# Kernel tuning notes

Measured on AMD Instinct MI355X. Metric: run time of the kernel, lower is better.

## Reference

```python
import jax, jax.numpy as jnp
import numpy as np

B, S, D = 4, 2048, 512
H = 8
HD = D // H  # 64


def setup_inputs() -> dict:
    key = jax.random.key(0)
    ks = jax.random.split(key, 11)
    scale = 1.0 / np.sqrt(D)
    inp = {
        "query": jax.random.normal(ks[0], (B, S, D), dtype=jnp.float32),
        "key": jax.random.normal(ks[1], (B, S, D), dtype=jnp.float32),
        "value": jax.random.normal(ks[2], (B, S, D), dtype=jnp.float32),
        "Wq": jax.random.normal(ks[3], (D, D), dtype=jnp.float32) * scale,
        "bq": jnp.zeros((D,), dtype=jnp.float32),
        "Wk": jax.random.normal(ks[4], (D, D), dtype=jnp.float32) * scale,
        "bk": jnp.zeros((D,), dtype=jnp.float32),
        "Wv": jax.random.normal(ks[5], (D, D), dtype=jnp.float32) * scale,
        "bv": jnp.zeros((D,), dtype=jnp.float32),
        "Wo": jax.random.normal(ks[6], (D, D), dtype=jnp.float32) * scale,
        "bo": jnp.zeros((D,), dtype=jnp.float32),
    }
    return inp


def reference(query, key, value, Wq, bq, Wk, bk, Wv, bv, Wo, bo):
    # Linear projections (torch Linear: x @ W.T + b)
    q = (query @ Wq.T + bq).reshape(B, -1, H, HD).transpose(0, 2, 1, 3)  # [B,H,Sq,HD]
    k = (key   @ Wk.T + bk).reshape(B, -1, H, HD).transpose(0, 2, 1, 3)  # [B,H,Sk,HD]
    v = (value @ Wv.T + bv).reshape(B, -1, H, HD).transpose(0, 2, 1, 3)  # [B,H,Sk,HD]

    # Chunked loop in original is mathematically identical to full attention
    scores = jnp.einsum('bhqd,bhkd->bhqk', q, k) / np.sqrt(HD)  # [B,H,Sq,Sk]
    attn = jax.nn.softmax(scores, axis=-1)
    out = jnp.einsum('bhqk,bhkd->bhqd', attn, v)  # [B,H,Sq,HD]
    out = out.transpose(0, 2, 1, 3).reshape(B, -1, D)  # [B,Sq,D]
    return out @ Wo.T + bo
```

## Files before the change

### kernel.cpp

```cpp
#include <hip/hip_runtime.h>
#include <hip/hip_bf16.h>

typedef __attribute__((ext_vector_type(8))) short bf16x8;
typedef __attribute__((ext_vector_type(4))) float f32x4;
typedef __attribute__((ext_vector_type(16))) float f32x16;
typedef __attribute__((ext_vector_type(4))) unsigned int u32x4;

#define MFMA16(a, b, c) __builtin_amdgcn_mfma_f32_16x16x32_bf16((a), (b), (c), 0, 0, 0)
#define MFMA32(a, b, c) __builtin_amdgcn_mfma_f32_32x32x16_bf16((a), (b), (c), 0, 0, 0)

static constexpr int BATCH = 4, S = 2048, DMODEL = 512, H = 8, HD = 64;
static constexpr int M = BATCH * S;

#define WAIT_VM(N) asm volatile("s_waitcnt vmcnt(" #N ")" ::: "memory")
#define WAIT_VM_LGKM(N) asm volatile("s_waitcnt vmcnt(" #N ") lgkmcnt(0)" ::: "memory")
#define SCHEDB() __builtin_amdgcn_sched_barrier(0)

__device__ __forceinline__ float rexp2(float x) {
  float r;
  asm("v_exp_f32 %0, %1" : "=v"(r) : "v"(x));
  return r;
}

__device__ __forceinline__ short f2b(float f) {
  unsigned int u = __builtin_bit_cast(unsigned int, f);
  unsigned int r = (u + 0x7fffu + ((u >> 16) & 1u)) >> 16;
  return (short)r;
}

__device__ __forceinline__ bf16x8 cvt8(const float4& a, const float4& b) {
  bf16x8 r;
  r[0] = f2b(a.x); r[1] = f2b(a.y); r[2] = f2b(a.z); r[3] = f2b(a.w);
  r[4] = f2b(b.x); r[5] = f2b(b.y); r[6] = f2b(b.z); r[7] = f2b(b.w);
  return r;
}

__device__ __forceinline__ void glds16(const void* g, void* l) {
  __builtin_amdgcn_global_load_lds(
      (const __attribute__((address_space(1))) unsigned int*)g,
      (__attribute__((address_space(3))) unsigned int*)l, 16, 0, 0);
}

__global__ __launch_bounds__(256) void convert_w(
    const float* __restrict__ Wq, const float* __restrict__ Wk,
    const float* __restrict__ Wv, const float* __restrict__ Wo,
    short* __restrict__ Wb) {
  const float* src = (blockIdx.y == 0) ? Wq : (blockIdx.y == 1) ? Wk
                   : (blockIdx.y == 2) ? Wv : Wo;
  short* dst = Wb + blockIdx.y * (DMODEL * DMODEL);
  int i = (blockIdx.x * 256 + threadIdx.x) * 8;
  float4 a = *(const float4*)&src[i];
  float4 b = *(const float4*)&src[i + 4];
  *(bf16x8*)&dst[i] = cvt8(a, b);
}

__global__ __launch_bounds__(256) void proj_gemm(
    const float* __restrict__ Aq, const float* __restrict__ Ak, const float* __restrict__ Av,
    const short* __restrict__ Wb,
    const float* __restrict__ bq, const float* __restrict__ bk, const float* __restrict__ bv,
    short* __restrict__ Qp, short* __restrict__ Kp, short* __restrict__ Vp) {
  const int which = blockIdx.y;
  const float* A    = (which == 0) ? Aq : (which == 1) ? Ak : Av;
  const short* W    = Wb + which * (DMODEL * DMODEL);
  const float* bias = (which == 0) ? bq : (which == 1) ? bk : bv;
  short* dst        = (which == 0) ? Qp : (which == 1) ? Kp : Vp;

  const int tm = blockIdx.x & 63;
  const int tn = blockIdx.x >> 6;
  const int m0 = tm * 128, n0 = tn * 128;
  const int t = threadIdx.x;
  const int lane = t & 63, w = t >> 6;
  const int g = lane >> 4, c = lane & 15;
  const int wr = w >> 1, wc = w & 1;

  __shared__ __align__(16) short As[2][128 * 32];
  __shared__ __align__(16) short Bs[3][128 * 32];

  f32x4 acc[4][4];
  const f32x4 fz = {0.f, 0.f, 0.f, 0.f};
#pragma unroll
  for (int i = 0; i < 4; ++i)
#pragma unroll
    for (int j = 0; j < 4; ++j) acc[i][j] = fz;

  const int r0 = t >> 2, c0 = (t & 3) * 8;
  const int r1 = r0 + 64;

  const short* Bsrc0 = W + (n0 + w * 16 + (lane >> 2)) * DMODEL + (lane & 3) * 8;
  const short* Bsrc1 = Bsrc0 + 64 * DMODEL;

  {
    float4 a0 = *(const float4*)&A[(m0 + r0) * DMODEL + c0];
    float4 a1 = *(const float4*)&A[(m0 + r0) * DMODEL + c0 + 4];
    float4 a2 = *(const float4*)&A[(m0 + r1) * DMODEL + c0];
    float4 a3 = *(const float4*)&A[(m0 + r1) * DMODEL + c0 + 4];
    glds16(Bsrc0, &Bs[0][w * 512]);
    glds16(Bsrc1, &Bs[0][2048 + w * 512]);
    glds16(Bsrc0 + 32, &Bs[1][w * 512]);
    glds16(Bsrc1 + 32, &Bs[1][2048 + w * 512]);
    *(bf16x8*)&As[0][r0 * 32 + c0] = cvt8(a0, a1);
    *(bf16x8*)&As[0][r1 * 32 + c0] = cvt8(a2, a3);
  }

  int ob0 = 0, ob1 = 1, ob2 = 2;
  for (int kt = 0; kt < 16; ++kt) {
    if (kt == 15) { WAIT_VM_LGKM(0); } else { WAIT_VM_LGKM(2); }
    __builtin_amdgcn_s_barrier();
    SCHEDB();

    float4 a0, a1, a2, a3;
    if (kt < 15) {
      const int k0 = (kt + 1) * 32;
      a0 = *(const float4*)&A[(m0 + r0) * DMODEL + k0 + c0];
      a1 = *(const float4*)&A[(m0 + r0) * DMODEL + k0 + c0 + 4];
      a2 = *(const float4*)&A[(m0 + r1) * DMODEL + k0 + c0];
      a3 = *(const float4*)&A[(m0 + r1) * DMODEL + k0 + c0 + 4];
    }
    if (kt < 14) {
      const int k0 = (kt + 2) * 32;
      glds16(Bsrc0 + k0, &Bs[ob2][w * 512]);
      glds16(Bsrc1 + k0, &Bs[ob2][2048 + w * 512]);
    }
    SCHEDB();

    bf16x8 af[4], bfr[4];
#pragma unroll
    for (int i = 0; i < 4; ++i)
      af[i] = *(const bf16x8*)&As[kt & 1][(wr * 64 + i * 16 + c) * 32 + g * 8];
#pragma unroll
    for (int j = 0; j < 4; ++j)
      bfr[j] = *(const bf16x8*)&Bs[ob0][(wc * 64 + j * 16 + c) * 32 + g * 8];
    if (which == 2) {
#pragma unroll
      for (int i = 0; i < 4; ++i)
#pragma unroll
        for (int j = 0; j < 4; ++j)
          acc[i][j] = MFMA16(bfr[j], af[i], acc[i][j]);
    } else {
#pragma unroll
      for (int i = 0; i < 4; ++i)
#pragma unroll
        for (int j = 0; j < 4; ++j)
          acc[i][j] = MFMA16(af[i], bfr[j], acc[i][j]);
    }

    if (kt < 15) {
      *(bf16x8*)&As[(kt + 1) & 1][r0 * 32 + c0] = cvt8(a0, a1);
      *(bf16x8*)&As[(kt + 1) & 1][r1 * 32 + c0] = cvt8(a2, a3);
    }
    const int tmp = ob0; ob0 = ob1; ob1 = ob2; ob2 = tmp;
  }

  if (which == 2) {
#pragma unroll
    for (int j = 0; j < 4; ++j) {
#pragma unroll
      for (int r = 0; r < 4; ++r) {
        const int n = n0 + wc * 64 + j * 16 + g * 4 + r;
        const int h = n >> 6, hd = n & 63;
        const float bn = bias[n];
#pragma unroll
        for (int i = 0; i < 4; ++i) {
          const int m = m0 + wr * 64 + i * 16 + c;
          const int bb = m >> 11, s = m & (S - 1);
          dst[((bb * H + h) * HD + hd) * S + s] = f2b(acc[i][j][r] + bn);
        }
      }
    }
  } else {
#pragma unroll
    for (int i = 0; i < 4; ++i) {
#pragma unroll
      for (int j = 0; j < 4; ++j) {
        const int n = n0 + wc * 64 + j * 16 + c;
        const int h = n >> 6, hd = n & 63;
        const float bn = bias[n];
#pragma unroll
        for (int r = 0; r < 4; ++r) {
          const int m = m0 + wr * 64 + i * 16 + g * 4 + r;
          const int bb = m >> 11, s = m & (S - 1);
          dst[((bb * H + h) * S + s) * HD + hd] = f2b(acc[i][j][r] + bn);
        }
      }
    }
  }
}

__global__ __launch_bounds__(256) void out_gemm(
    const short* __restrict__ Am, const short* __restrict__ W,
    const float* __restrict__ bias, float* __restrict__ Out) {
  const int tm = blockIdx.x & 63;
  const int tn = blockIdx.x >> 6;
  const int m0 = tm * 128, n0 = tn * 128;
  const int t = threadIdx.x;
  const int lane = t & 63, w = t >> 6;
  const int g = lane >> 4, c = lane & 15;
  const int wr = w >> 1, wc = w & 1;

  __shared__ __align__(16) short SM[3][2 * 128 * 32];

  f32x4 acc[4][4];
  const f32x4 fz = {0.f, 0.f, 0.f, 0.f};
#pragma unroll
  for (int i = 0; i < 4; ++i)
#pragma unroll
    for (int j = 0; j < 4; ++j) acc[i][j] = fz;

  const short* Asrc0 = Am + (m0 + w * 16 + (lane >> 2)) * DMODEL + (lane & 3) * 8;
  const short* Asrc1 = Asrc0 + 64 * DMODEL;
  const short* Bsrc0 = W + (n0 + w * 16 + (lane >> 2)) * DMODEL + (lane & 3) * 8;
  const short* Bsrc1 = Bsrc0 + 64 * DMODEL;

#pragma unroll
  for (int tt = 0; tt < 2; ++tt) {
    glds16(Asrc0 + tt * 32, &SM[tt][w * 512]);
    glds16(Asrc1 + tt * 32, &SM[tt][2048 + w * 512]);
    glds16(Bsrc0 + tt * 32, &SM[tt][4096 + w * 512]);
    glds16(Bsrc1 + tt * 32, &SM[tt][4096 + 2048 + w * 512]);
  }

  int ob0 = 0, ob1 = 1, ob2 = 2;
  for (int kt = 0; kt < 16; ++kt) {
    if (kt == 15) { WAIT_VM(0); } else { WAIT_VM(4); }
    __builtin_amdgcn_s_barrier();
    SCHEDB();
    if (kt < 14) {
      const int k0 = (kt + 2) * 32;
      glds16(Asrc0 + k0, &SM[ob2][w * 512]);
      glds16(Asrc1 + k0, &SM[ob2][2048 + w * 512]);
      glds16(Bsrc0 + k0, &SM[ob2][4096 + w * 512]);
      glds16(Bsrc1 + k0, &SM[ob2][4096 + 2048 + w * 512]);
    }
    SCHEDB();

    bf16x8 af[4], bfr[4];
#pragma unroll
    for (int i = 0; i < 4; ++i)
      af[i] = *(const bf16x8*)&SM[ob0][(wr * 64 + i * 16 + c) * 32 + g * 8];
#pragma unroll
    for (int j = 0; j < 4; ++j)
      bfr[j] = *(const bf16x8*)&SM[ob0][4096 + (wc * 64 + j * 16 + c) * 32 + g * 8];
#pragma unroll
    for (int i = 0; i < 4; ++i)
#pragma unroll
      for (int j = 0; j < 4; ++j)
        acc[i][j] = MFMA16(af[i], bfr[j], acc[i][j]);

    const int tmp = ob0; ob0 = ob1; ob1 = ob2; ob2 = tmp;
  }

#pragma unroll
  for (int i = 0; i < 4; ++i) {
#pragma unroll
    for (int j = 0; j < 4; ++j) {
      const int n = n0 + wc * 64 + j * 16 + c;
      const float bn = bias[n];
#pragma unroll
      for (int r = 0; r < 4; ++r) {
        const int m = m0 + wr * 64 + i * 16 + g * 4 + r;
        Out[m * DMODEL + n] = acc[i][j][r] + bn;
      }
    }
  }
}

__global__ __launch_bounds__(256, 2) void attn_kernel(
    const short* __restrict__ Qp, const short* __restrict__ Kp,
    const short* __restrict__ VTp, short* __restrict__ att) {
  const int bid = blockIdx.x;
  const int swzb = (bid & 7) * 64 + (bid >> 3);
  const int qt = swzb & 15;
  const int bh = swzb >> 4;
  const int b = bh >> 3, h = bh & 7;
  const short* Q  = Qp  + bh * (S * HD);
  const char*  Kg = (const char*)(Kp  + bh * (S * HD));
  const char*  Vg = (const char*)(VTp + bh * (HD * S));

  const int t = threadIdx.x;
  const int lane = t & 63, w = t >> 6;
  const int l31 = lane & 31, hi = lane >> 5;
  const int q0 = qt * 128 + w * 32;

  __shared__ __align__(16) char smem[2 * 32768];

  const int rowi = lane >> 3;
  const char* ksrc = Kg + (w * 32 + rowi) * 128 + (((lane & 7) * 16) ^ (rowi << 4));
  const int vrow = lane >> 4;
  const char* vsrc[4];
#pragma unroll
  for (int j = 0; j < 4; ++j)
    vsrc[j] = Vg + (w * 16 + j * 4 + vrow) * 4096 +
              (((lane & 15) * 16) ^ (((j * 4 + vrow) & 7) << 4));

  bf16x8 qf[4];
#pragma unroll
  for (int ks = 0; ks < 4; ++ks)
    qf[ks] = *(const bf16x8*)&Q[(q0 + l31) * HD + ks * 16 + hi * 8];

  bf16x8 ones;
#pragma unroll
  for (int i = 0; i < 8; ++i) ones[i] = (short)0x3F80;

  f32x16 o0, o1, osum, fz16;
#pragma unroll
  for (int i = 0; i < 16; ++i) { o0[i] = 0.f; o1[i] = 0.f; osum[i] = 0.f; fz16[i] = 0.f; }

  const float SCL = 0.18033688011112042f;
  const int fswz = (l31 & 7) << 4;

  {
    char* nb = smem;
#pragma unroll
    for (int j = 0; j < 4; ++j) glds16(ksrc + j * 1024, nb + w * 4096 + j * 1024);
#pragma unroll
    for (int j = 0; j < 4; ++j) glds16(vsrc[j], nb + 16384 + w * 4096 + j * 1024);
  }

  for (int kt = 0; kt < 16; ++kt) {
    WAIT_VM(0);
    __builtin_amdgcn_s_barrier();
    SCHEDB();
    if (kt < 15) {
      char* nb = smem + ((kt + 1) & 1) * 32768;
      const size_t ko = (size_t)(kt + 1) * 16384;
      const size_t vo = (size_t)(kt + 1) * 256;
#pragma unroll
      for (int j = 0; j < 4; ++j) glds16(ksrc + ko + j * 1024, nb + w * 4096 + j * 1024);
#pragma unroll
      for (int j = 0; j < 4; ++j) glds16(vsrc[j] + vo, nb + 16384 + w * 4096 + j * 1024);
    }
    SCHEDB();

    const int cb = (kt & 1) * 32768;
#pragma unroll
    for (int hb = 0; hb < 2; ++hb) {
      const int kvb = cb + hb * 64 * 128;
      f32x16 sa0, sa1;
      __builtin_amdgcn_s_setprio(1);
      {
        const int col0 = (hi * 16) ^ fswz;
        const bf16x8 k00 = *(const bf16x8*)&smem[kvb + l31 * 128 + col0];
        const bf16x8 k10 = *(const bf16x8*)&smem[kvb + (32 + l31) * 128 + col0];
        sa0 = MFMA32(k00, qf[0], fz16);
        sa1 = MFMA32(k10, qf[0], fz16);
      }
#pragma unroll
      for (int ks = 1; ks < 4; ++ks) {
        const int col = (ks * 32 + hi * 16) ^ fswz;
        const bf16x8 k0 = *(const bf16x8*)&smem[kvb + l31 * 128 + col];
        const bf16x8 k1 = *(const bf16x8*)&smem[kvb + (32 + l31) * 128 + col];
        sa0 = MFMA32(k0, qf[ks], sa0);
        sa1 = MFMA32(k1, qf[ks], sa1);
      }
      __builtin_amdgcn_s_setprio(0);

#pragma unroll
      for (int i = 0; i < 16; ++i) {
        sa0[i] = rexp2(sa0[i] * SCL);
        sa1[i] = rexp2(sa1[i] * SCL);
      }

      unsigned int wrd0[8], wrd1[8];
#pragma unroll
      for (int i = 0; i < 8; ++i) {
        asm("v_cvt_pk_bf16_f32 %0, %1, %2" : "=v"(wrd0[i]) : "v"(sa0[2 * i]), "v"(sa0[2 * i + 1]));
        asm("v_cvt_pk_bf16_f32 %0, %1, %2" : "=v"(wrd1[i]) : "v"(sa1[2 * i]), "v"(sa1[2 * i + 1]));
      }

      __builtin_amdgcn_s_setprio(1);
#pragma unroll
      for (int ks = 0; ks < 4; ++ks) {
        const int i0 = (ks & 1) * 4;
        unsigned int a0 = (ks < 2) ? wrd0[i0 + 0] : wrd1[i0 + 0];
        unsigned int b0 = (ks < 2) ? wrd0[i0 + 2] : wrd1[i0 + 2];
        unsigned int a1 = (ks < 2) ? wrd0[i0 + 1] : wrd1[i0 + 1];
        unsigned int b1 = (ks < 2) ? wrd0[i0 + 3] : wrd1[i0 + 3];
        asm("v_permlane32_swap_b32 %0, %1" : "+v"(a0), "+v"(b0));
        asm("v_permlane32_swap_b32 %0, %1" : "+v"(a1), "+v"(b1));
        u32x4 fw;
        fw[0] = a0; fw[1] = a1; fw[2] = b0; fw[3] = b1;
        const bf16x8 pfrag = __builtin_bit_cast(bf16x8, fw);
        const int colv = (hb * 128 + ks * 32 + hi * 16) ^ fswz;
        const bf16x8 va0 = *(const bf16x8*)&smem[cb + 16384 + l31 * 256 + colv];
        const bf16x8 va1 = *(const bf16x8*)&smem[cb + 16384 + (32 + l31) * 256 + colv];
        o0 = MFMA32(va0, pfrag, o0);
        o1 = MFMA32(va1, pfrag, o1);
        osum = MFMA32(ones, pfrag, osum);
      }
      __builtin_amdgcn_s_setprio(0);
    }
  }

  const float inv = 1.0f / osum[0];
  short* arow = att + (b * S + q0 + l31) * DMODEL + h * HD;
#pragma unroll
  for (int dt = 0; dt < 2; ++dt) {
#pragma unroll
    for (int rr = 0; rr < 4; ++rr) {
      float v0 = (dt ? o1[4 * rr + 0] : o0[4 * rr + 0]) * inv;
      float v1 = (dt ? o1[4 * rr + 1] : o0[4 * rr + 1]) * inv;
      float v2 = (dt ? o1[4 * rr + 2] : o0[4 * rr + 2]) * inv;
      float v3 = (dt ? o1[4 * rr + 3] : o0[4 * rr + 3]) * inv;
      unsigned int w0, w1;
      asm("v_cvt_pk_bf16_f32 %0, %1, %2" : "=v"(w0) : "v"(v0), "v"(v1));
      asm("v_cvt_pk_bf16_f32 %0, %1, %2" : "=v"(w1) : "v"(v2), "v"(v3));
      uint2 pk2;
      pk2.x = w0; pk2.y = w1;
      *(uint2*)&arow[dt * 32 + rr * 8 + hi * 4] = pk2;
    }
  }
}

extern "C" void kernel_launch(void* const* d_in, const int* in_sizes, int n_in,
                              void* d_out, int out_size, void* d_ws, size_t ws_size,
                              hipStream_t stream) {
  const float* query = (const float*)d_in[0];
  const float* key_  = (const float*)d_in[1];
  const float* value = (const float*)d_in[2];
  const float* Wq = (const float*)d_in[3];
  const float* bq = (const float*)d_in[4];
  const float* Wk = (const float*)d_in[5];
  const float* bk = (const float*)d_in[6];
  const float* Wv = (const float*)d_in[7];
  const float* bv = (const float*)d_in[8];
  const float* Wo = (const float*)d_in[9];
  const float* bo = (const float*)d_in[10];
  float* out = (float*)d_out;

  char* ws = (char*)d_ws;
  const size_t WB_BYTES  = (size_t)4 * DMODEL * DMODEL * 2;
  const size_t MAT_BYTES = (size_t)M * DMODEL * 2;
  short* Wb  = (short*)ws;
  short* Qp  = (short*)(ws + WB_BYTES);
  short* Kp  = (short*)(ws + WB_BYTES + MAT_BYTES);
  short* Vp  = (short*)(ws + WB_BYTES + 2 * MAT_BYTES);
  short* att = (short*)(ws + WB_BYTES + 3 * MAT_BYTES);

  convert_w<<<dim3(128, 4), 256, 0, stream>>>(Wq, Wk, Wv, Wo, Wb);
  proj_gemm<<<dim3(256, 3), 256, 0, stream>>>(query, key_, value, Wb, bq, bk, bv, Qp, Kp, Vp);
  attn_kernel<<<dim3(512), 256, 0, stream>>>(Qp, Kp, Vp, att);
  out_gemm<<<dim3(256), 256, 0, stream>>>(att, Wb + 3 * DMODEL * DMODEL, bo, out);
}
```

Baseline: 103.8 us.

## Deepen projection GEMM prefetch to two k-steps for both A and B tiles

The projection GEMM now issues the fp32 A-tile global loads two k-steps ahead, using register double-buffering, instead of one step ahead. The B ring in LDS grows from three to four buffers, indexed by kt&3, and the vmcnt wait is relaxed from 2 to 6 outstanding loads. The loop is unrolled by four and launch bounds request three blocks per SM. The aim is to hide global-load latency; the cost is more live registers and more LDS, which could limit occupancy or cause spills.

```diff
diff --git a/kernel.cpp b/kernel.cpp
--- a/kernel.cpp
+++ b/kernel.cpp
@@ -54,7 +54,7 @@
   *(bf16x8*)&dst[i] = cvt8(a, b);
 }
 
-__global__ __launch_bounds__(256) void proj_gemm(
+__global__ __launch_bounds__(256, 3) void proj_gemm(
     const float* __restrict__ Aq, const float* __restrict__ Ak, const float* __restrict__ Av,
     const short* __restrict__ Wb,
     const float* __restrict__ bq, const float* __restrict__ bk, const float* __restrict__ bv,
@@ -74,7 +74,7 @@
   const int wr = w >> 1, wc = w & 1;
 
   __shared__ __align__(16) short As[2][128 * 32];
-  __shared__ __align__(16) short Bs[3][128 * 32];
+  __shared__ __align__(16) short Bs[4][128 * 32];
 
   f32x4 acc[4][4];
   const f32x4 fz = {0.f, 0.f, 0.f, 0.f};
@@ -85,41 +85,45 @@
 
   const int r0 = t >> 2, c0 = (t & 3) * 8;
   const int r1 = r0 + 64;
+  const float* Ar0 = A + (m0 + r0) * DMODEL + c0;
+  const float* Ar1 = A + (m0 + r1) * DMODEL + c0;
 
   const short* Bsrc0 = W + (n0 + w * 16 + (lane >> 2)) * DMODEL + (lane & 3) * 8;
   const short* Bsrc1 = Bsrc0 + 64 * DMODEL;
 
+  float4 ap0, ap1, ap2, ap3;
   {
-    float4 a0 = *(const float4*)&A[(m0 + r0) * DMODEL + c0];
-    float4 a1 = *(const float4*)&A[(m0 + r0) * DMODEL + c0 + 4];
-    float4 a2 = *(const float4*)&A[(m0 + r1) * DMODEL + c0];
-    float4 a3 = *(const float4*)&A[(m0 + r1) * DMODEL + c0 + 4];
+    float4 q0 = *(const float4*)&Ar0[0];
+    float4 q1 = *(const float4*)&Ar0[4];
+    float4 q2 = *(const float4*)&Ar1[0];
+    float4 q3 = *(const float4*)&Ar1[4];
+    *(bf16x8*)&As[0][r0 * 32 + c0] = cvt8(q0, q1);
+    *(bf16x8*)&As[0][r1 * 32 + c0] = cvt8(q2, q3);
     glds16(Bsrc0, &Bs[0][w * 512]);
     glds16(Bsrc1, &Bs[0][2048 + w * 512]);
     glds16(Bsrc0 + 32, &Bs[1][w * 512]);
     glds16(Bsrc1 + 32, &Bs[1][2048 + w * 512]);
-    *(bf16x8*)&As[0][r0 * 32 + c0] = cvt8(a0, a1);
-    *(bf16x8*)&As[0][r1 * 32 + c0] = cvt8(a2, a3);
-  }
-
-  int ob0 = 0, ob1 = 1, ob2 = 2;
+    ap0 = *(const float4*)&Ar0[32];
+    ap1 = *(const float4*)&Ar0[36];
+    ap2 = *(const float4*)&Ar1[32];
+    ap3 = *(const float4*)&Ar1[36];
+  }
+
+#pragma unroll 4
   for (int kt = 0; kt < 16; ++kt) {
-    if (kt == 15) { WAIT_VM_LGKM(0); } else { WAIT_VM_LGKM(2); }
+    if (kt == 15) { WAIT_VM_LGKM(0); } else { WAIT_VM_LGKM(6); }
     __builtin_amdgcn_s_barrier();
     SCHEDB();
 
-    float4 a0, a1, a2, a3;
-    if (kt < 15) {
-      const int k0 = (kt + 1) * 32;
-      a0 = *(const float4*)&A[(m0 + r0) * DMODEL + k0 + c0];
-      a1 = *(const float4*)&A[(m0 + r0) * DMODEL + k0 + c0 + 4];
-      a2 = *(const float4*)&A[(m0 + r1) * DMODEL + k0 + c0];
-      a3 = *(const float4*)&A[(m0 + r1) * DMODEL + k0 + c0 + 4];
-    }
-    if (kt < 14) {
+    float4 an0, an1, an2, an3;
+    if (kt <= 13) {
       const int k0 = (kt + 2) * 32;
-      glds16(Bsrc0 + k0, &Bs[ob2][w * 512]);
-      glds16(Bsrc1 + k0, &Bs[ob2][2048 + w * 512]);
+      glds16(Bsrc0 + k0, &Bs[(kt + 2) & 3][w * 512]);
+      glds16(Bsrc1 + k0, &Bs[(kt + 2) & 3][2048 + w * 512]);
+      an0 = *(const float4*)&Ar0[k0];
+      an1 = *(const float4*)&Ar0[k0 + 4];
+      an2 = *(const float4*)&Ar1[k0];
+      an3 = *(const float4*)&Ar1[k0 + 4];
     }
     SCHEDB();
 
@@ -129,7 +133,7 @@
       af[i] = *(const bf16x8*)&As[kt & 1][(wr * 64 + i * 16 + c) * 32 + g * 8];
 #pragma unroll
     for (int j = 0; j < 4; ++j)
-      bfr[j] = *(const bf16x8*)&Bs[ob0][(wc * 64 + j * 16 + c) * 32 + g * 8];
+      bfr[j] = *(const bf16x8*)&Bs[kt & 3][(wc * 64 + j * 16 + c) * 32 + g * 8];
     if (which == 2) {
 #pragma unroll
       for (int i = 0; i < 4; ++i)
@@ -144,11 +148,11 @@
           acc[i][j] = MFMA16(af[i], bfr[j], acc[i][j]);
     }
 
-    if (kt < 15) {
-      *(bf16x8*)&As[(kt + 1) & 1][r0 * 32 + c0] = cvt8(a0, a1);
-      *(bf16x8*)&As[(kt + 1) & 1][r1 * 32 + c0] = cvt8(a2, a3);
-    }
-    const int tmp = ob0; ob0 = ob1; ob1 = ob2; ob2 = tmp;
+    if (kt <= 14) {
+      *(bf16x8*)&As[(kt + 1) & 1][r0 * 32 + c0] = cvt8(ap0, ap1);
+      *(bf16x8*)&As[(kt + 1) & 1][r1 * 32 + c0] = cvt8(ap2, ap3);
+    }
+    ap0 = an0; ap1 = an1; ap2 = an2; ap3 = an3;
   }
 
   if (which == 2) {
```

Result: slower. 162.2 us (+56.2%).

## Pre-convert activations to bf16 and stream both GEMM operands via direct-to-LDS loads

Applied to the files above, without the earlier changes.

Activations are now converted from fp32 to bf16 in a merged conversion kernel along with the weights, instead of being converted inside the projection GEMM. The projection GEMM then loads both A and B tiles asynchronously with global_load_lds into a 3-stage shared buffer, which removes the register round-trip and the in-loop conversion. The trade-off is an extra full pass over the activations: one fp32 read plus one bf16 write and a later bf16 re-read. The V activation buffer reuses the attention output workspace.

```diff
diff --git a/kernel.cpp b/kernel.cpp
--- a/kernel.cpp
+++ b/kernel.cpp
@@ -13,7 +13,6 @@
 static constexpr int M = BATCH * S;
 
 #define WAIT_VM(N) asm volatile("s_waitcnt vmcnt(" #N ")" ::: "memory")
-#define WAIT_VM_LGKM(N) asm volatile("s_waitcnt vmcnt(" #N ") lgkmcnt(0)" ::: "memory")
 #define SCHEDB() __builtin_amdgcn_sched_barrier(0)
 
 __device__ __forceinline__ float rexp2(float x) {
@@ -41,26 +40,42 @@
       (__attribute__((address_space(3))) unsigned int*)l, 16, 0, 0);
 }
 
-__global__ __launch_bounds__(256) void convert_w(
+__global__ __launch_bounds__(256) void convert_all(
+    const float* __restrict__ q, const float* __restrict__ k, const float* __restrict__ v,
     const float* __restrict__ Wq, const float* __restrict__ Wk,
     const float* __restrict__ Wv, const float* __restrict__ Wo,
+    short* __restrict__ Abq, short* __restrict__ Abk, short* __restrict__ Abv,
     short* __restrict__ Wb) {
-  const float* src = (blockIdx.y == 0) ? Wq : (blockIdx.y == 1) ? Wk
-                   : (blockIdx.y == 2) ? Wv : Wo;
-  short* dst = Wb + blockIdx.y * (DMODEL * DMODEL);
-  int i = (blockIdx.x * 256 + threadIdx.x) * 8;
+  const int bid = blockIdx.x;
+  const float* src;
+  short* dst;
+  int i;
+  if (bid < 6144) {
+    const int which = bid >> 11;
+    const int sub = bid & 2047;
+    src = (which == 0) ? q : (which == 1) ? k : v;
+    dst = (which == 0) ? Abq : (which == 1) ? Abk : Abv;
+    i = (sub * 256 + threadIdx.x) * 8;
+  } else {
+    const int wb = bid - 6144;
+    const int which = wb >> 7;
+    const int sub = wb & 127;
+    src = (which == 0) ? Wq : (which == 1) ? Wk : (which == 2) ? Wv : Wo;
+    dst = Wb + which * (DMODEL * DMODEL);
+    i = (sub * 256 + threadIdx.x) * 8;
+  }
   float4 a = *(const float4*)&src[i];
   float4 b = *(const float4*)&src[i + 4];
   *(bf16x8*)&dst[i] = cvt8(a, b);
 }
 
 __global__ __launch_bounds__(256) void proj_gemm(
-    const float* __restrict__ Aq, const float* __restrict__ Ak, const float* __restrict__ Av,
+    const short* __restrict__ Abq, const short* __restrict__ Abk, const short* __restrict__ Abv,
     const short* __restrict__ Wb,
     const float* __restrict__ bq, const float* __restrict__ bk, const float* __restrict__ bv,
     short* __restrict__ Qp, short* __restrict__ Kp, short* __restrict__ Vp) {
   const int which = blockIdx.y;
-  const float* A    = (which == 0) ? Aq : (which == 1) ? Ak : Av;
+  const short* A    = (which == 0) ? Abq : (which == 1) ? Abk : Abv;
   const short* W    = Wb + which * (DMODEL * DMODEL);
   const float* bias = (which == 0) ? bq : (which == 1) ? bk : bv;
   short* dst        = (which == 0) ? Qp : (which == 1) ? Kp : Vp;
@@ -73,8 +88,7 @@
   const int g = lane >> 4, c = lane & 15;
   const int wr = w >> 1, wc = w & 1;
 
-  __shared__ __align__(16) short As[2][128 * 32];
-  __shared__ __align__(16) short Bs[3][128 * 32];
+  __shared__ __align__(16) short SM[3][2 * 128 * 32];
 
   f32x4 acc[4][4];
   const f32x4 fz = {0.f, 0.f, 0.f, 0.f};
@@ -83,53 +97,40 @@
 #pragma unroll
     for (int j = 0; j < 4; ++j) acc[i][j] = fz;
 
-  const int r0 = t >> 2, c0 = (t & 3) * 8;
-  const int r1 = r0 + 64;
-
+  const short* Asrc0 = A + (m0 + w * 16 + (lane >> 2)) * DMODEL + (lane & 3) * 8;
+  const short* Asrc1 = Asrc0 + 64 * DMODEL;
   const short* Bsrc0 = W + (n0 + w * 16 + (lane >> 2)) * DMODEL + (lane & 3) * 8;
   const short* Bsrc1 = Bsrc0 + 64 * DMODEL;
 
-  {
-    float4 a0 = *(const float4*)&A[(m0 + r0) * DMODEL + c0];
-    float4 a1 = *(const float4*)&A[(m0 + r0) * DMODEL + c0 + 4];
-    float4 a2 = *(const float4*)&A[(m0 + r1) * DMODEL + c0];
-    float4 a3 = *(const float4*)&A[(m0 + r1) * DMODEL + c0 + 4];
-    glds16(Bsrc0, &Bs[0][w * 512]);
-    glds16(Bsrc1, &Bs[0][2048 + w * 512]);
-    glds16(Bsrc0 + 32, &Bs[1][w * 512]);
-    glds16(Bsrc1 + 32, &Bs[1][2048 + w * 512]);
-    *(bf16x8*)&As[0][r0 * 32 + c0] = cvt8(a0, a1);
-    *(bf16x8*)&As[0][r1 * 32 + c0] = cvt8(a2, a3);
+#pragma unroll
+  for (int tt = 0; tt < 2; ++tt) {
+    glds16(Asrc0 + tt * 32, &SM[tt][w * 512]);
+    glds16(Asrc1 + tt * 32, &SM[tt][2048 + w * 512]);
+    glds16(Bsrc0 + tt * 32, &SM[tt][4096 + w * 512]);
+    glds16(Bsrc1 + tt * 32, &SM[tt][4096 + 2048 + w * 512]);
   }
 
   int ob0 = 0, ob1 = 1, ob2 = 2;
   for (int kt = 0; kt < 16; ++kt) {
-    if (kt == 15) { WAIT_VM_LGKM(0); } else { WAIT_VM_LGKM(2); }
+    if (kt == 15) { WAIT_VM(0); } else { WAIT_VM(4); }
     __builtin_amdgcn_s_barrier();
     SCHEDB();
-
-    float4 a0, a1, a2, a3;
-    if (kt < 15) {
-      const int k0 = (kt + 1) * 32;
-      a0 = *(const float4*)&A[(m0 + r0) * DMODEL + k0 + c0];
-      a1 = *(const float4*)&A[(m0 + r0) * DMODEL + k0 + c0 + 4];
-      a2 = *(const float4*)&A[(m0 + r1) * DMODEL + k0 + c0];
-      a3 = *(const float4*)&A[(m0 + r1) * DMODEL + k0 + c0 + 4];
-    }
     if (kt < 14) {
       const int k0 = (kt + 2) * 32;
-      glds16(Bsrc0 + k0, &Bs[ob2][w * 512]);
-      glds16(Bsrc1 + k0, &Bs[ob2][2048 + w * 512]);
+      glds16(Asrc0 + k0, &SM[ob2][w * 512]);
+      glds16(Asrc1 + k0, &SM[ob2][2048 + w * 512]);
+      glds16(Bsrc0 + k0, &SM[ob2][4096 + w * 512]);
+      glds16(Bsrc1 + k0, &SM[ob2][4096 + 2048 + w * 512]);
     }
     SCHEDB();
 
     bf16x8 af[4], bfr[4];
 #pragma unroll
     for (int i = 0; i < 4; ++i)
-      af[i] = *(const bf16x8*)&As[kt & 1][(wr * 64 + i * 16 + c) * 32 + g * 8];
+      af[i] = *(const bf16x8*)&SM[ob0][(wr * 64 + i * 16 + c) * 32 + g * 8];
 #pragma unroll
     for (int j = 0; j < 4; ++j)
-      bfr[j] = *(const bf16x8*)&Bs[ob0][(wc * 64 + j * 16 + c) * 32 + g * 8];
+      bfr[j] = *(const bf16x8*)&SM[ob0][4096 + (wc * 64 + j * 16 + c) * 32 + g * 8];
     if (which == 2) {
 #pragma unroll
       for (int i = 0; i < 4; ++i)
@@ -144,10 +145,6 @@
           acc[i][j] = MFMA16(af[i], bfr[j], acc[i][j]);
     }
 
-    if (kt < 15) {
-      *(bf16x8*)&As[(kt + 1) & 1][r0 * 32 + c0] = cvt8(a0, a1);
-      *(bf16x8*)&As[(kt + 1) & 1][r1 * 32 + c0] = cvt8(a2, a3);
-    }
     const int tmp = ob0; ob0 = ob1; ob1 = ob2; ob2 = tmp;
   }
 
@@ -435,9 +432,13 @@
   short* Kp  = (short*)(ws + WB_BYTES + MAT_BYTES);
   short* Vp  = (short*)(ws + WB_BYTES + 2 * MAT_BYTES);
   short* att = (short*)(ws + WB_BYTES + 3 * MAT_BYTES);
-
-  convert_w<<<dim3(128, 4), 256, 0, stream>>>(Wq, Wk, Wv, Wo, Wb);
-  proj_gemm<<<dim3(256, 3), 256, 0, stream>>>(query, key_, value, Wb, bq, bk, bv, Qp, Kp, Vp);
+  short* Abq = (short*)(ws + WB_BYTES + 4 * MAT_BYTES);
+  short* Abk = (short*)(ws + WB_BYTES + 5 * MAT_BYTES);
+  short* Abv = att;
+
+  convert_all<<<dim3(6656), 256, 0, stream>>>(query, key_, value, Wq, Wk, Wv, Wo,
+                                              Abq, Abk, Abv, Wb);
+  proj_gemm<<<dim3(256, 3), 256, 0, stream>>>(Abq, Abk, Abv, Wb, bq, bk, bv, Qp, Kp, Vp);
   attn_kernel<<<dim3(512), 256, 0, stream>>>(Qp, Kp, Vp, att);
   out_gemm<<<dim3(256), 256, 0, stream>>>(att, Wb + 3 * DMODEL * DMODEL, bo, out);
 }
```

Measured after the change: 95.06 us. 1.09x faster.
